# Optimization experiments

Measured on AMD Instinct MI355X. Metric: run time of the kernel, lower is better.

Reference implementation:

```python
import jax, jax.numpy as jnp
import numpy as np

V, K, D, T, B, M = 32000, 32, 256, 128, 128, 16
NEG = -1e9


def setup_inputs():
    key = jax.random.key(0)
    ks = jax.random.split(key, 32)
    def rn(k, shape):
        return (0.05 * jax.random.normal(k, shape)).astype(jnp.float32)
    u = jax.random.uniform(ks[4], (T, B, K), minval=1e-6, maxval=1.0 - 1e-6)
    return dict(
        keys=jax.random.randint(ks[0], (B, M), 1, V),
        vals=jax.random.randint(ks[1], (B, M), 1, V),
        sentences=jax.random.randint(ks[2], (B, T), 1, V),
        sent_lens=jax.random.randint(ks[3], (B,), T // 2, T + 1),
        tau=jnp.float32(0.5),
        x_lambd=jnp.float32(0.5),
        gumbel_noise=(-jnp.log(-jnp.log(u))).astype(jnp.float32),
        drop_unif=jax.random.uniform(ks[5], (B, T)).astype(jnp.float32),
        emb=rn(ks[6], (V, D)), z_emb=rn(ks[7], (K, D)),
        enc_Wih=rn(ks[8], (D, 4 * D)), enc_Whh=rn(ks[9], (D, 4 * D)), enc_b=jnp.zeros((4 * D,), jnp.float32),
        crf_W=rn(ks[10], (D, K)), crf_b=jnp.zeros((K,), jnp.float32), crf_trans=rn(ks[11], (K, K)),
        init_Wh=rn(ks[12], (D, D)), init_bh=jnp.zeros((D,), jnp.float32),
        init_Wc=rn(ks[13], (D, D)), init_bc=jnp.zeros((D,), jnp.float32),
        dec_Wih=rn(ks[14], (D, 4 * D)), dec_Whh=rn(ks[15], (D, 4 * D)), dec_b=jnp.zeros((4 * D,), jnp.float32),
        attn_Wq=rn(ks[16], (D, D)), attn_Wk=rn(ks[17], (D, D)), attn_v=rn(ks[18], (D,)),
        attn_out_W=rn(ks[19], (2 * D, D)), attn_out_b=jnp.zeros((D,), jnp.float32),
        pz_W=rn(ks[20], (D, K)), pz_b=jnp.zeros((K,), jnp.float32),
        int_W=rn(ks[21], (2 * D, D)), int_b=jnp.zeros((D,), jnp.float32),
        out_W=rn(ks[22], (D, V)), out_b=jnp.zeros((V,), jnp.float32),
        cattn_Wq=rn(ks[23], (D, D)), cattn_Wk=rn(ks[24], (D, D)), cattn_v=rn(ks[25], (D,)),
        g_W=rn(ks[26], (D, 1)), g_b=jnp.zeros((1,), jnp.float32),
    )


def _lstm_step(h, c, x, Wih, Whh, b):
    g = x @ Wih + h @ Whh + b
    i, f, gg, o = jnp.split(g, 4, axis=-1)
    c = jax.nn.sigmoid(f) * c + jax.nn.sigmoid(i) * jnp.tanh(gg)
    h = jax.nn.sigmoid(o) * jnp.tanh(c)
    return h, c


def _attend(q, memk, mem_vals, mask, v):
    # additive attention: q [B,D], memk = mem @ Wk [B,M,D]
    e = jnp.einsum('bmd,d->bm', jnp.tanh(q[:, None, :] + memk), v)
    e = jnp.where(mask, e, NEG)
    a = jax.nn.softmax(e, axis=-1)
    ctx = jnp.einsum('bm,bmd->bd', a, mem_vals)
    return ctx, a


def _forward(tau, x_lambd, gumbel_noise, drop_unif, emb, z_emb,
             enc_Wih, enc_Whh, enc_b, crf_W, crf_b, crf_trans,
             init_Wh, init_bh, init_Wc, init_bc,
             dec_Wih, dec_Whh, dec_b,
             attn_Wq, attn_Wk, attn_v, attn_out_W, attn_out_b,
             pz_W, pz_b, int_W, int_b, out_W, out_b,
             cattn_Wq, cattn_Wk, cattn_v, g_W, g_b,
             keys, vals, sentences, sent_lens):
    z_beta = 1.0
    lens = sent_lens
    # ---- q encoder: 1-layer LSTM over sentence embeddings ----
    sent_emb = emb[sentences]                            # [B,T,D]
    def enc_step(carry, x_t):
        h, c = _lstm_step(carry[0], carry[1], x_t, enc_Wih, enc_Whh, enc_b)
        return (h, c), h
    z0 = jnp.zeros((B, D), jnp.float32)
    _, enc_out = jax.lax.scan(enc_step, (z0, z0), sent_emb.transpose(1, 0, 2))
    enc_out = enc_out.transpose(1, 0, 2)                 # [B,T,D]
    # ---- emission scores with overlap logits ----
    phi = enc_out @ crf_W + crf_b                        # [B,T,K]
    phi = phi.at[:, :-1].add(phi[:, 1:])                 # scores[:,:-1] += scores[:,1:].clone()
    phi = phi.at[:, 1:].add(phi[:, :-1])                 # scores[:,1:]  += scores[:,:-1].clone()
    # ---- linear-chain CRF forward recursion: alpha + exact entropy ----
    phiT = phi.transpose(1, 0, 2)                        # [T,B,K]
    def crf_step(carry, inputs):
        alpha, H = carry
        phi_t, t = inputs
        scores = alpha[:, :, None] + crf_trans[None]     # [B,Ki,Kj]
        lZ = jax.nn.logsumexp(scores, axis=1)            # [B,Kj]
        logw = scores - lZ[:, None, :]
        w = jnp.exp(logw)
        na = lZ + phi_t
        nH = jnp.sum(w * (H[:, :, None] - logw), axis=1)
        m = (t < lens)[:, None]
        na = jnp.where(m, na, alpha)
        nH = jnp.where(m, nH, H)
        return (na, nH), na
    (aT, HT), alphas = jax.lax.scan(
        crf_step, (phiT[0], jnp.zeros((B, K), jnp.float32)),
        (phiT[1:], jnp.arange(1, T)))
    alphas = jnp.concatenate([phiT[0][None], alphas], axis=0)   # [T,B,K]
    logp_last = jax.nn.log_softmax(aT, axis=-1)
    ent_z = jnp.mean(jnp.sum(jnp.exp(logp_last) * (HT - logp_last), axis=-1))
    # ---- Gumbel FFBS backward sampling ----
    def bwd_step(nid, inputs):
        alpha_t, g_t, t = inputs
        is_last = (t == lens - 1)[:, None]
        active = (t < lens)
        logits = jnp.where(is_last, alpha_t, alpha_t + crf_trans[:, nid].T)
        y = jax.nn.softmax((logits + g_t) / tau, axis=-1)
        y = jnp.where(active[:, None], y, 0.0)
        ids = jnp.where(active, jnp.argmax(y, axis=-1).astype(jnp.int32), 0)
        return ids, (ids, y)
    ts = jnp.arange(T)
    _, (ids_r, y_r) = jax.lax.scan(
        bwd_step, jnp.zeros((B,), jnp.int32),
        (alphas[::-1], gumbel_noise[::-1], ts[::-1]))
    z_ids = ids_r[::-1].transpose(1, 0)                  # [B,T]
    z_sample = y_r[::-1].transpose(1, 0, 2)              # [B,T,K]
    z_sample_emb = z_sample @ z_emb                      # soft gumbel encode [B,T,D]
    # ---- key-value table encoding ----
    kv_mask = keys != 0
    kv_emb = emb[keys] + emb[vals]                       # [B,M,D]
    kvm = kv_mask.astype(jnp.float32)
    kv_enc = (kv_emb * kvm[..., None]).sum(1) / kvm.sum(1, keepdims=True)
    # ---- decoder io (word dropout x_lambd, z[0] zeroed) ----
    zse = z_sample_emb.at[:, 0].multiply(0.0)
    wmask = (drop_unif > x_lambd).astype(jnp.float32)[..., None]
    dec_inputs = (zse + sent_emb * wmask)[:, :-1]        # [B,T-1,D]
    tgt_x = sentences[:, 1:]
    tgt_z = z_ids[:, 1:]
    z_next = z_sample_emb[:, 1:]
    h0 = kv_enc @ init_Wh + init_bh
    c0 = kv_enc @ init_Wc + init_bc
    memk = kv_emb @ attn_Wk
    memk2 = kv_emb @ cattn_Wk
    rows = jnp.arange(B)
    def dec_step(carry, inputs):
        h, c = carry
        x_t, zn_t, tx, tz = inputs
        h, c = _lstm_step(h, c, x_t, dec_Wih, dec_Whh, dec_b)
        ctx, _ = _attend(h @ attn_Wq, memk, kv_emb, kv_mask, attn_v)
        dec_out = jnp.concatenate([h, ctx], axis=-1) @ attn_out_W + attn_out_b
        z_logits = dec_out @ pz_W + pz_b
        lpz = jnp.take_along_axis(jax.nn.log_softmax(z_logits, -1), tz[:, None], 1)[:, 0]
        dec_int = jnp.concatenate([dec_out, zn_t], axis=-1) @ int_W + int_b
        lm_prob = jax.nn.softmax(dec_int @ out_W + out_b, axis=-1)       # [B,V]
        _, copy_dist = _attend(dec_int @ cattn_Wq, memk2, kv_emb, kv_mask, cattn_v)
        copy_prob = jnp.zeros((B, V), lm_prob.dtype).at[rows[:, None], keys].add(copy_dist)
        g = jax.nn.sigmoid(dec_int @ g_W + g_b)                           # [B,1]
        out_prob = (1.0 - g) * lm_prob + g * copy_prob
        lpx = jnp.log(jnp.take_along_axis(out_prob, tx[:, None], 1)[:, 0] + 1e-10)
        return (h, c), (lpx, lpz)
    _, (lpx, lpz) = jax.lax.scan(
        dec_step, (h0, c0),
        (dec_inputs.transpose(1, 0, 2), z_next.transpose(1, 0, 2),
         tgt_x.transpose(1, 0), tgt_z.transpose(1, 0)))
    steps = jnp.arange(T - 1)
    smask = (steps[None, :] < lens[:, None]).astype(jnp.float32)
    denom = jnp.sum(lens).astype(jnp.float32)
    p_log_prob = (jnp.sum(lpx.transpose(1, 0) * smask) + jnp.sum(lpz.transpose(1, 0) * smask)) / denom
    loss = -(z_beta * ent_z + p_log_prob)
    return loss


def reference(keys, vals, sentences, sent_lens, tau, x_lambd, gumbel_noise,
              drop_unif, emb, z_emb, enc_Wih, enc_Whh, enc_b, crf_W, crf_b,
              crf_trans, init_Wh, init_bh, init_Wc, init_bc, dec_Wih, dec_Whh,
              dec_b, attn_Wq, attn_Wk, attn_v, attn_out_W, attn_out_b, pz_W,
              pz_b, int_W, int_b, out_W, out_b, cattn_Wq, cattn_Wk, cattn_v,
              g_W, g_b):
    return _forward(tau, x_lambd, gumbel_noise, drop_unif, emb, z_emb,
                    enc_Wih, enc_Whh, enc_b, crf_W, crf_b, crf_trans,
                    init_Wh, init_bh, init_Wc, init_bc, dec_Wih, dec_Whh,
                    dec_b, attn_Wq, attn_Wk, attn_v, attn_out_W, attn_out_b,
                    pz_W, pz_b, int_W, int_b, out_W, out_b,
                    cattn_Wq, cattn_Wk, cattn_v, g_W, g_b,
                    keys, vals, sentences, sent_lens)
```

## Files before the change

### kernel.cpp

```cpp
#include <hip/hip_runtime.h>
#include <math.h>

namespace {

constexpr int V_  = 32000;
constexpr int K_  = 32;
constexpr int D_  = 256;
constexpr int T_  = 128;
constexpr int B_  = 128;
constexpr int M_  = 16;
constexpr int D4_ = 1024;
constexpr int TD_ = T_ - 1;
constexpr int R_  = B_ * TD_;
constexpr int NCH_ = 8;

typedef __attribute__((ext_vector_type(8))) short short8;
typedef __attribute__((ext_vector_type(4))) float f32x4;
typedef __attribute__((ext_vector_type(2))) float f32x2;

__device__ __forceinline__ float d_rcp(float x){
#if __has_builtin(__builtin_amdgcn_rcpf)
  return __builtin_amdgcn_rcpf(x);
#else
  return 1.0f / x;
#endif
}
__device__ __forceinline__ float d_sig(float x){
  return d_rcp(1.0f + __expf(-x));
}
__device__ __forceinline__ float d_tanh(float x){
  float e = __expf(2.0f*x);
  return 1.0f - 2.0f*d_rcp(e + 1.0f);
}
__device__ __forceinline__ unsigned short f2bf(float f){
  unsigned int x = __float_as_uint(f);
  unsigned int r = (x + 0x7FFFu + ((x>>16)&1u)) >> 16;
  return (unsigned short)r;
}
__device__ __forceinline__ float bflo(unsigned u){ return __uint_as_float(u<<16); }
__device__ __forceinline__ float bfhi(unsigned u){ return __uint_as_float(u & 0xffff0000u); }

__device__ __forceinline__ unsigned f2fp8(float f){
  unsigned u = __float_as_uint(f);
  unsigned s = (u>>31)<<7;
  float a = fabsf(f);
  if (a < 0.015625f){
    int m = (int)rintf(a*512.0f);
    if (m >= 8) return s | 0x08u;
    return s | (unsigned)m;
  }
  unsigned t = u & 0x7FFFFFFFu;
  t += 0x7FFFFu + ((t>>20)&1u);
  int E = (int)(t>>23) - 127 + 7;
  if (E >= 16) return s | 0x7Eu;
  return s | ((unsigned)E<<3) | ((t>>20)&7u);
}

__device__ __forceinline__ unsigned pack4_fp8(float a, float b, float c, float d){
#if __has_builtin(__builtin_amdgcn_cvt_pk_fp8_f32)
  unsigned r = (unsigned)__builtin_amdgcn_cvt_pk_fp8_f32(a, b, 0, false);
  r = (unsigned)__builtin_amdgcn_cvt_pk_fp8_f32(c, d, (int)r, true);
  return r;
#else
  return f2fp8(a) | (f2fp8(b)<<8) | (f2fp8(c)<<16) | (f2fp8(d)<<24);
#endif
}
__device__ __forceinline__ unsigned char f2fp8_b(float f){
#if __has_builtin(__builtin_amdgcn_cvt_pk_fp8_f32)
  return (unsigned char)(__builtin_amdgcn_cvt_pk_fp8_f32(f, f, 0, false) & 0xFF);
#else
  return (unsigned char)f2fp8(f);
#endif
}

__device__ __forceinline__ void cvt4_fp8(unsigned w, float* o){
#if __has_builtin(__builtin_amdgcn_cvt_pk_f32_fp8)
  f32x2 lo = __builtin_amdgcn_cvt_pk_f32_fp8(w, false);
  f32x2 hi = __builtin_amdgcn_cvt_pk_f32_fp8(w, true);
  o[0]=lo.x; o[1]=lo.y; o[2]=hi.x; o[3]=hi.y;
#else
  #pragma unroll
  for (int j = 0; j < 4; j++){
    unsigned b = (w>>(8*j)) & 0xFFu;
    unsigned e = (b>>3) & 15u, m = b & 7u;
    float mag = e ? __uint_as_float(((e+120u)<<23)|(m<<20)) : (float)m*0.001953125f;
    o[j] = (b & 0x80u) ? -mag : mag;
  }
#endif
}

__global__ void k_sent_emb(const int* __restrict__ sent, const float* __restrict__ emb,
                           float* __restrict__ out){
  int idx = blockIdx.x*256 + threadIdx.x;
  int bt = idx >> 8, d = idx & 255;
  out[idx] = emb[(size_t)sent[bt]*D_ + d];
}

__global__ void k_kv_emb(const int* __restrict__ keys, const int* __restrict__ vals,
                         const float* __restrict__ emb, float* __restrict__ kv){
  int idx = blockIdx.x*256 + threadIdx.x;
  int r = idx >> 8, d = idx & 255;
  kv[idx] = emb[(size_t)keys[r]*D_ + d] + emb[(size_t)vals[r]*D_ + d];
}

__global__ void k_kv_enc(const int* __restrict__ keys, const float* __restrict__ kv,
                         float* __restrict__ out){
  int idx = blockIdx.x*256 + threadIdx.x;
  int b = idx >> 8, d = idx & 255;
  float s = 0.0f, c = 0.0f;
  for (int m = 0; m < M_; m++){
    if (keys[b*M_+m] != 0){ s += kv[(size_t)(b*M_+m)*D_ + d]; c += 1.0f; }
  }
  out[idx] = s / c;
}

__global__ void k_rowgemm(const float* __restrict__ A, const float* __restrict__ W,
                          const float* __restrict__ bias, float* __restrict__ C,
                          int inner, int cols){
  __shared__ float sA[256];
  int r = blockIdx.x;
  if ((int)threadIdx.x < inner) sA[threadIdx.x] = A[(size_t)r*inner + threadIdx.x];
  __syncthreads();
  for (int j = threadIdx.x; j < cols; j += blockDim.x){
    float acc = bias ? bias[j] : 0.0f;
    #pragma unroll 4
    for (int d = 0; d < inner; d++) acc += sA[d]*W[(size_t)d*cols + j];
    C[(size_t)r*cols + j] = acc;
  }
}

__global__ __launch_bounds__(256) void k_wt8(const float* __restrict__ W,
                                             unsigned char* __restrict__ Wt8, int ldw){
  __shared__ unsigned char st[64][272];
  int tid = threadIdx.x; size_t c0 = (size_t)blockIdx.x*64;
  for (int l = tid; l < 64*256; l += 256){
    int k = l >> 6, c = l & 63;
    st[c][k] = f2fp8_b(W[(size_t)k*ldw + c0 + c]);
  }
  __syncthreads();
  for (int l = tid; l < 64*16; l += 256){
    int c = l >> 4, s = l & 15;
    *reinterpret_cast<uint4*>(&Wt8[(c0+c)*256 + s*16]) =
      *reinterpret_cast<const uint4*>(&st[c][s*16]);
  }
}

__global__ __launch_bounds__(256) void k_wtg(const float* __restrict__ W,
                                             unsigned short* __restrict__ Wt, int ldw){
  __shared__ unsigned short st[64][264];
  int tid = threadIdx.x; size_t c0 = (size_t)blockIdx.x*64;
  for (int l = tid; l < 64*256; l += 256){
    int k = l >> 6, c = l & 63;
    st[c][k] = f2bf(W[(size_t)k*ldw + c0 + c]);
  }
  __syncthreads();
  for (int l = tid; l < 64*32; l += 256){
    int c = l >> 5, s = l & 31;
    *reinterpret_cast<uint4*>(&Wt[(c0+c)*256 + s*8]) =
      *reinterpret_cast<const uint4*>(&st[c][s*8]);
  }
}

__global__ __launch_bounds__(256) void k_wtg6(
    const float* s0, const float* s1, const float* s2,
    const float* s3, const float* s4, const float* s5,
    unsigned short* d0, unsigned short* d1, unsigned short* d2,
    unsigned short* d3, unsigned short* d4, unsigned short* d5){
  __shared__ unsigned short st[64][264];
  int m = blockIdx.x >> 2, blk = blockIdx.x & 3;
  const float* S; unsigned short* D;
  if      (m == 0){ S = s0; D = d0; }
  else if (m == 1){ S = s1; D = d1; }
  else if (m == 2){ S = s2; D = d2; }
  else if (m == 3){ S = s3; D = d3; }
  else if (m == 4){ S = s4; D = d4; }
  else            { S = s5; D = d5; }
  int tid = threadIdx.x; size_t c0 = (size_t)blk*64;
  for (int l = tid; l < 64*256; l += 256){
    int k = l >> 6, c = l & 63;
    st[c][k] = f2bf(S[(size_t)k*256 + c0 + c]);
  }
  __syncthreads();
  for (int l = tid; l < 64*32; l += 256){
    int c = l >> 5, s = l & 31;
    *reinterpret_cast<uint4*>(&D[(c0+c)*256 + s*8]) =
      *reinterpret_cast<const uint4*>(&st[c][s*8]);
  }
}

template<int G1, int G2, int HALVES, int CPB, bool BIAS, int TMD>
__global__ __launch_bounds__(512) void k_gemm(
    const float* __restrict__ A1, const float* __restrict__ A2,
    const unsigned short* __restrict__ W1, const unsigned short* __restrict__ W2,
    const float* __restrict__ bias, float* __restrict__ C, int cols,
    const float* __restrict__ drop, const float* __restrict__ xl){
  __shared__ unsigned short Al[128*256];
  __shared__ unsigned short Wl[64*256];
  int tid = threadIdx.x;
  int row0 = blockIdx.x*128;
  int w = tid >> 6, l = tid & 63;
  int arow = 16*w + (l & 15);
  float xlv = 0.0f;
  if constexpr (G1==1) xlv = xl[0];
  f32x4 acc[CPB][4];
  #pragma unroll
  for (int cc=0;cc<CPB;cc++)
    #pragma unroll
    for (int nf=0;nf<4;nf++) acc[cc][nf] = (f32x4){0.f,0.f,0.f,0.f};

  for (int h = 0; h < HALVES; h++){
    const float* Asrc = h ? A2 : A1;
    const unsigned short* Wt = h ? W2 : W1;
    int gm = h ? G2 : G1;
    __syncthreads();
    #pragma unroll
    for (int q = 0; q < 8; q++){
      int u = tid + q*512;
      int row = u >> 5, slot = u & 31;
      int r = row0 + row;
      float vals[8];
      if (gm == 0){
        const float* s = Asrc + (size_t)r*256 + slot*8;
        #pragma unroll
        for (int j=0;j<8;j++) vals[j] = s[j];
      } else if (gm == 1){
        int b = r / TD_, t = r - b*TD_;
        int bt = b*T_ + t;
        float wm = (drop[bt] > xlv) ? 1.0f : 0.0f;
        const float* se = A1 + (size_t)bt*256 + slot*8;
        const float* zs = A2 + (size_t)bt*256 + slot*8;
        #pragma unroll
        for (int j=0;j<8;j++) vals[j] = se[j]*wm + (t>0 ? zs[j] : 0.0f);
      } else {
        int b = r / TD_, t = r - b*TD_;
        const float* s = Asrc + (size_t)(b*T_ + t + 1)*256 + slot*8;
        #pragma unroll
        for (int j=0;j<8;j++) vals[j] = s[j];
      }
      union { unsigned short us[8]; uint4 v4; } tu;
      #pragma unroll
      for (int j=0;j<8;j++) tu.us[j] = f2bf(vals[j]);
// ... 38 lines not shown
  for (int cc = 0; cc < CPB; cc++){
    int col0 = (blockIdx.y*CPB + cc)*64;
    #pragma unroll
    for (int nf = 0; nf < 4; nf++){
      int col = col0 + nf*16 + (l & 15);
      float bv = BIAS ? bias[col] : 0.0f;
      #pragma unroll
      for (int r4 = 0; r4 < 4; r4++){
        int row = row0 + 16*w + (l>>4)*4 + r4;
        size_t orow;
        if constexpr (TMD == 0){
          orow = (size_t)row;
        } else {
          int bb = row / TMD, tt = row - bb*TMD;
          orow = (size_t)tt*B_ + bb;
        }
        C[orow*cols + col] = acc[cc][nf][r4] + bv;
      }
    }
  }
}

__global__ __launch_bounds__(1024, 4) void k_lstm12(
    const float* __restrict__ xW,
    const unsigned char* __restrict__ Wt,
    const float* __restrict__ h0, const float* __restrict__ c0,
    float* __restrict__ Hout,
    int NT){
  __shared__ unsigned char Wl[512*256];
  __shared__ unsigned char Ahl[2][16*256];
  int g0 = blockIdx.x;
  int tid = threadIdx.x;
  int w = tid >> 6, l = tid & 63;

  for (int i = tid; i < 512*16; i += 1024){
    int c = i >> 4, s16 = i & 15;
    int dst = c*256 + ((s16*16) ^ ((c&7)<<4));
    *reinterpret_cast<uint4*>(&Wl[dst]) =
      *reinterpret_cast<const uint4*>(&Wt[(size_t)c*256 + s16*16]);
  }
  if (tid < 256){
    int row = tid >> 4, gblk = tid & 15;
    unsigned pk[4];
    #pragma unroll
    for (int g = 0; g < 4; g++){
      float v0 = h0 ? h0[(size_t)(g0*16+row)*256 + gblk*16 + 4*g + 0] : 0.0f;
      float v1 = h0 ? h0[(size_t)(g0*16+row)*256 + gblk*16 + 4*g + 1] : 0.0f;
      float v2 = h0 ? h0[(size_t)(g0*16+row)*256 + gblk*16 + 4*g + 2] : 0.0f;
      float v3 = h0 ? h0[(size_t)(g0*16+row)*256 + gblk*16 + 4*g + 3] : 0.0f;
      pk[g] = pack4_fp8(v0, v1, v2, v3);
    }
    int dst = row*256 + ((gblk*16) ^ ((row&7)<<4));
    *reinterpret_cast<uint4*>(&Ahl[0][dst]) = *reinterpret_cast<const uint4*>(pk);
  }
  int cb = 16*w + (l & 15);
  int arow = l & 15;
  float creg[4];
  #pragma unroll
  for (int r = 0; r < 4; r++)
    creg[r] = c0 ? c0[(size_t)(g0*16 + (l>>4)*4 + r)*256 + cb] : 0.0f;

  int aoff[8], b0off[8], b1off[8];
  #pragma unroll
  for (int k0 = 0; k0 < 8; k0++){
    int kb = k0*32 + ((l>>4)*8);
    aoff[k0]  = arow*256 + (kb ^ ((arow&7)<<4));
    b0off[k0] = cb*256 + (kb ^ ((cb&7)<<4));
    b1off[k0] = (256+cb)*256 + (kb ^ ((cb&7)<<4));
  }
  const unsigned char* wg2 = Wt + (size_t)(512+cb)*256 + ((l>>4)*8);
  const unsigned char* wg3 = Wt + (size_t)(768+cb)*256 + ((l>>4)*8);
  int astore[4];
  const float* xb[4];
  float* hp[4];
  #pragma unroll
  for (int r = 0; r < 4; r++){
    int batch = (l>>4)*4 + r;
    astore[r] = batch*256 + ((cb & 0xF0) ^ ((batch&7)<<4)) + (cb & 15);
    xb[r] = xW + (size_t)(g0*16 + batch)*1024 + cb;
    hp[r] = Hout + (size_t)(g0*16 + batch)*NT*256 + cb;
  }
  __syncthreads();

  float xn[4][4];
  #pragma unroll
  for (int gt = 0; gt < 4; gt++)
    #pragma unroll
    for (int r = 0; r < 4; r++)
      xn[gt][r] = xb[r][gt*256];

  for (int t = 0; t < NT; t++){
    int cur = t & 1, nxt = cur ^ 1;
    f32x4 acc[4];
    #pragma unroll
    for (int gt = 0; gt < 4; gt++)
      #pragma unroll
      for (int r = 0; r < 4; r++)
        acc[gt][r] = xn[gt][r];
    if (t + 1 < NT){
      #pragma unroll
      for (int r = 0; r < 4; r++) xb[r] += B_*1024;
      #pragma unroll
      for (int gt = 0; gt < 4; gt++)
        #pragma unroll
        for (int r = 0; r < 4; r++)
          xn[gt][r] = xb[r][gt*256];
    }
    const unsigned char* Ac = Ahl[cur];
    #pragma unroll
    for (int k0 = 0; k0 < 8; k0++){
      long long afr = *reinterpret_cast<const long long*>(Ac + aoff[k0]);
      long long b0 = *reinterpret_cast<const long long*>(Wl + b0off[k0]);
      long long b1 = *reinterpret_cast<const long long*>(Wl + b1off[k0]);
      long long b2 = *reinterpret_cast<const long long*>(wg2 + k0*32);
      long long b3 = *reinterpret_cast<const long long*>(wg3 + k0*32);
      acc[0] = __builtin_amdgcn_mfma_f32_16x16x32_fp8_fp8(afr, b0, acc[0], 0, 0, 0);
      acc[1] = __builtin_amdgcn_mfma_f32_16x16x32_fp8_fp8(afr, b1, acc[1], 0, 0, 0);
      acc[2] = __builtin_amdgcn_mfma_f32_16x16x32_fp8_fp8(afr, b2, acc[2], 0, 0, 0);
      acc[3] = __builtin_amdgcn_mfma_f32_16x16x32_fp8_fp8(afr, b3, acc[3], 0, 0, 0);
    }
    #pragma unroll
    for (int r = 0; r < 4; r++){
      float vi = acc[0][r], vf = acc[1][r];
      float vg = acc[2][r], vo = acc[3][r];
      float cn = d_sig(vf)*creg[r] + d_sig(vi)*d_tanh(vg);
      float hn = d_sig(vo)*d_tanh(cn);
      creg[r] = cn;
      Ahl[nxt][astore[r]] = f2fp8_b(hn);
      hp[r][0] = hn;
      hp[r] += 256;
    }
    __syncthreads();
  }
}

__global__ __launch_bounds__(256) void k_phi(const float* __restrict__ H,
    const float* __restrict__ Wc, const float* __restrict__ bc,
    float* __restrict__ phi){
  int tid = threadIdx.x; int rl = tid >> 5, j = tid & 31;
  int r = blockIdx.x*8 + rl;
  int b = r >> 7, t = r & 127;
  float acc = bc[j];
  #pragma unroll 4
  for (int d = 0; d < 256; d++) acc += H[(size_t)r*256 + d]*Wc[d*K_ + j];
  phi[(size_t)t*B_*K_ + b*K_ + j] = acc;
}

__global__ __launch_bounds__(256) void k_zlp(const float* __restrict__ A,
    const float* __restrict__ Wz, const float* __restrict__ bz,
    const int* __restrict__ zids, float* __restrict__ lpz){
  int tid = threadIdx.x; int rl = tid >> 5, j = tid & 31;
  int r = blockIdx.x*8 + rl;
  float acc = bz[j];
  #pragma unroll 4
  for (int d = 0; d < 256; d++) acc += A[(size_t)r*256 + d]*Wz[d*K_ + j];
  float m = acc;
  #pragma unroll
  for (int off=16; off; off>>=1) m = fmaxf(m, __shfl_xor(m, off, 32));
  float e = __expf(acc - m), E = e;
  #pragma unroll
  for (int off=16; off; off>>=1) E += __shfl_xor(E, off, 32);
  int b = r / TD_, t = r - b*TD_;
  int tz = zids[b*T_ + t + 1];
  float vtz = __shfl(acc, tz, 32);
  if (j == 0) lpz[r] = vtz - (m + logf(E));
}

__global__ __launch_bounds__(1024) void k_crf(
    const float* __restrict__ phi, const float* __restrict__ trans,
    const int* __restrict__ lens, float* __restrict__ alphas,
    float* __restrict__ ent_b){
  __shared__ float sal[K_], sH[K_];
  int tid = threadIdx.x, b = blockIdx.x;
  int i = tid & 31, j = tid >> 5;
  float tr = trans[i*K_ + j];
  int len = lens[b];
  if (tid < K_){
    float a0 = phi[b*K_ + tid] + phi[(size_t)B_*K_ + b*K_ + tid];
    sal[tid] = a0; sH[tid] = 0.0f;
    alphas[b*K_ + tid] = a0;
  }
  __syncthreads();
  for (int t = 1; t < T_; t++){
    bool active = (t < len);
    float ai = sal[i], Hi = sH[i];
    float aj = sal[j], Hj = sH[j];
    float s = ai + tr;
    float m = s;
    #pragma unroll
    for (int off=16; off; off>>=1) m = fmaxf(m, __shfl_xor(m, off, 32));
    float e = expf(s - m);
    float E = e;
    #pragma unroll
    for (int off=16; off; off>>=1) E += __shfl_xor(E, off, 32);
    float lZ = m + logf(E);
    float w = e / E;
    float logw = s - lZ;
    float nH = w * (Hi - logw);
    #pragma unroll
    for (int off=16; off; off>>=1) nH += __shfl_xor(nH, off, 32);
    float pm = phi[(size_t)(t-1)*B_*K_ + b*K_ + j];
    float pt = phi[(size_t)t*B_*K_ + b*K_ + j];
    float ps = (t == T_-1) ? (pm + 2.0f*pt)
                           : (pm + 2.0f*pt + phi[(size_t)(t+1)*B_*K_ + b*K_ + j]);
    float na = lZ + ps;
    float outa = active ? na : aj;
    float outH = active ? nH : Hj;
    __syncthreads();
    if (i == 0){
      sal[j] = outa; sH[j] = outH;
      alphas[(size_t)t*B_*K_ + b*K_ + j] = outa;
    }
    __syncthreads();
  }
  if (tid < K_){
    float a = sal[tid];
    float m = a;
    #pragma unroll
    for (int off=16; off; off>>=1) m = fmaxf(m, __shfl_xor(m, off, 32));
    float e = expf(a-m), E = e;
    #pragma unroll
    for (int off=16; off; off>>=1) E += __shfl_xor(E, off, 32);
    float lse = m + logf(E);
    float lp = a - lse;
    float v = expf(lp)*(sH[tid]-lp);
    #pragma unroll
    for (int off=16; off; off>>=1) v += __shfl_xor(v, off, 32);
    if (tid == 0) ent_b[b] = v;
  }
}

__global__ void k_sampler(const float* __restrict__ alphas, const float* __restrict__ trans,
                          const float* __restrict__ gum, const int* __restrict__ lens,
                          const float* __restrict__ tau_p,
                          float* __restrict__ y_all, int* __restrict__ z_ids){
  int b = blockIdx.x;
  int lane = threadIdx.x;
  int k = lane & 31;
  float inv_tau = d_rcp(tau_p[0]);
  int len = lens[b];
  int nid = 0;
  for (int t = T_-1; t >= 0; t--){
    bool active  = (t < len);
    bool is_last = (t == len-1);
    float a = alphas[(size_t)t*B_*K_ + b*K_ + k];
    float lg = is_last ? a : a + trans[k*K_ + nid];
    float val = (lg + gum[(size_t)t*B_*K_ + b*K_ + k]) * inv_tau;
    float m = val;
    #pragma unroll
    for (int off=16; off; off>>=1) m = fmaxf(m, __shfl_xor(m, off, 32));
    float e = expf(val - m), E = e;
    #pragma unroll
    for (int off=16; off; off>>=1) E += __shfl_xor(E, off, 32);
    float y = active ? e*d_rcp(E) : 0.0f;
    if (lane < K_) y_all[(size_t)(b*T_ + t)*K_ + k] = y;
    float bv = val; int bk = k;
    #pragma unroll
    for (int off=16; off; off>>=1){
      float ov = __shfl_xor(bv, off, 32);
      int   ok = __shfl_xor(bk, off, 32);
      if (ov > bv || (ov == bv && ok < bk)){ bv = ov; bk = ok; }
    }
    int ids = active ? bk : 0;
    nid = ids;
    if (lane == 0) z_ids[b*T_ + t] = ids;
  }
}

__global__ __launch_bounds__(256) void k_attn1(
    const float* __restrict__ q, const float* __restrict__ memk,
    const float* __restrict__ kv_emb, const int* __restrict__ keys,
    const float* __restrict__ av, float* __restrict__ ctx){
  __shared__ float se[16];
  int r = blockIdx.x, tid = threadIdx.x;
  int b = r / TD_;
  int m = tid >> 4, ds = tid & 15;
  float p = 0.0f;
  #pragma unroll 4
  for (int qq = 0; qq < 16; qq++){
    int dd = ds + qq*16;
    p += d_tanh(q[(size_t)r*256 + dd] + memk[(size_t)(b*M_+m)*256 + dd]) * av[dd];
  }
  #pragma unroll
  for (int off=8; off; off>>=1) p += __shfl_xor(p, off, 16);
  if (ds == 0) se[m] = (keys[b*M_+m] != 0) ? p : -1e9f;
  __syncthreads();
  float mx = -1e30f;
  #pragma unroll
  for (int mm=0;mm<16;mm++) mx = fmaxf(mx, se[mm]);
  float den = 0.0f, ex[16];
  #pragma unroll
  for (int mm=0;mm<16;mm++){ ex[mm] = __expf(se[mm]-mx); den += ex[mm]; }
  float cacc = 0.0f;
  #pragma unroll
  for (int mm=0;mm<16;mm++) cacc += ex[mm]*kv_emb[(size_t)(b*M_+mm)*256 + tid];
  ctx[(size_t)r*256 + tid] = cacc*d_rcp(den);
}

__global__ __launch_bounds__(256) void k_attn2g(
    const float* __restrict__ q2, const float* __restrict__ dint,
    const float* __restrict__ memk2, const int* __restrict__ keys,
    const float* __restrict__ cv, const float* __restrict__ gW, const float* __restrict__ gb,
    const int* __restrict__ sent,
    float* __restrict__ cpx, float* __restrict__ gsig){
  __shared__ float se2[16];
  __shared__ float sred[4];
  int r = blockIdx.x, tid = threadIdx.x;
  int b = r / TD_, t = r - b*TD_;
  int m = tid >> 4, ds = tid & 15;
  float p = 0.0f;
  #pragma unroll 4
  for (int qq = 0; qq < 16; qq++){
    int dd = ds + qq*16;
    p += d_tanh(q2[(size_t)r*256 + dd] + memk2[(size_t)(b*M_+m)*256 + dd]) * cv[dd];
  }
  #pragma unroll
  for (int off=8; off; off>>=1) p += __shfl_xor(p, off, 16);
  if (ds == 0) se2[m] = (keys[b*M_+m] != 0) ? p : -1e9f;
  float gp = dint[(size_t)r*256 + tid]*gW[tid];
  #pragma unroll
  for (int off=32; off; off>>=1) gp += __shfl_xor(gp, off, 64);
  if ((tid & 63) == 0) sred[tid>>6] = gp;
  __syncthreads();
  if (tid == 0){
    float mx = -1e30f;
    #pragma unroll
    for (int mm=0;mm<16;mm++) mx = fmaxf(mx, se2[mm]);
    float den = 0.0f, ex[16];
    #pragma unroll
    for (int mm=0;mm<16;mm++){ ex[mm] = __expf(se2[mm]-mx); den += ex[mm]; }
    int txi = sent[b*T_ + t + 1];
    float idn = d_rcp(den);
    float cp = 0.0f;
    #pragma unroll
    for (int mm=0;mm<16;mm++) if (keys[b*M_+mm] == txi) cp += ex[mm]*idn;
    cpx[r] = cp;
    gsig[r] = d_sig(sred[0]+sred[1]+sred[2]+sred[3] + gb[0]);
  }
}

__global__ __launch_bounds__(512) void k_lse8(
    const float* __restrict__ Af,
    const unsigned char* __restrict__ Wt8,
    const float* __restrict__ bias,
    float* __restrict__ part){
  __shared__ unsigned char Al[256*256];
  __shared__ unsigned char Wl[64*256];
  int tid = threadIdx.x;
  int row0 = blockIdx.x*256;
  #pragma unroll
  for (int q = 0; q < 8; q++){
    int u = tid + q*512;
    int row = u >> 4, s16 = u & 15;
    int r = row0 + row;
    unsigned pk[4] = {0u,0u,0u,0u};
    if (r < R_){
      const float* src = Af + (size_t)r*256 + s16*16;
      #pragma unroll
      for (int g = 0; g < 4; g++){
        float4 f = *reinterpret_cast<const float4*>(src + g*4);
        pk[g] = pack4_fp8(f.x, f.y, f.z, f.w);
      }
    }
    int dst = row*256 + ((s16*16) ^ ((row&7)<<4));
    *reinterpret_cast<uint4*>(&Al[dst]) = *reinterpret_cast<const uint4*>(pk);
  }
  __syncthreads();
  int w = tid >> 6, l = tid & 63;
  int arow = 16*w + (l & 15);
  long long afrA[8], afrB[8];
  #pragma unroll
  for (int k0 = 0; k0 < 8; k0++){
    int kb = k0*32 + ((l>>4)*8);
    afrA[k0] = *reinterpret_cast<const long long*>(&Al[arow*256 + (kb ^ ((arow&7)<<4))]);
    int ar2 = arow + 128;
    afrB[k0] = *reinterpret_cast<const long long*>(&Al[ar2*256 + (kb ^ ((ar2&7)<<4))]);
  }
  float rm[2][4], rs[2][4];
  #pragma unroll
  for (int rf=0;rf<2;rf++)
    #pragma unroll
    for (int r4=0;r4<4;r4++){ rm[rf][r4] = -3.0e38f; rs[rf][r4] = 0.0f; }

  for (int ct = blockIdx.y; ct < 500; ct += NCH_){
    int col0 = ct*64;
    __syncthreads();
    #pragma unroll
    for (int q = 0; q < 2; q++){
      int u = tid + q*512;
      int c = u >> 4, s16 = u & 15;
      int dst = c*256 + ((s16*16) ^ ((c&7)<<4));
      *reinterpret_cast<uint4*>(&Wl[dst]) =
        *reinterpret_cast<const uint4*>(&Wt8[(size_t)(col0+c)*256 + s16*16]);
    }
    __syncthreads();
    f32x4 acc[2][4];
    #pragma unroll
    for (int rf=0;rf<2;rf++)
      #pragma unroll
      for (int nf=0;nf<4;nf++) acc[rf][nf] = (f32x4){0.f,0.f,0.f,0.f};
    #pragma unroll
    for (int k0 = 0; k0 < 8; k0++){
      int kb = k0*32 + ((l>>4)*8);
      #pragma unroll
      for (int nf = 0; nf < 4; nf++){
        int bc = nf*16 + (l & 15);
        long long bfr = *reinterpret_cast<const long long*>(&Wl[bc*256 + (kb ^ ((bc&7)<<4))]);
        acc[0][nf] = __builtin_amdgcn_mfma_f32_16x16x32_fp8_fp8(afrA[k0], bfr, acc[0][nf], 0, 0, 0);
        acc[1][nf] = __builtin_amdgcn_mfma_f32_16x16x32_fp8_fp8(afrB[k0], bfr, acc[1][nf], 0, 0, 0);
      }
    }
    float bb[4];
    #pragma unroll
    for (int nf=0;nf<4;nf++) bb[nf] = bias[col0 + nf*16 + (l&15)];
    #pragma unroll
    for (int rf = 0; rf < 2; rf++){
      #pragma unroll
      for (int r4 = 0; r4 < 4; r4++){
        float v0 = acc[rf][0][r4]+bb[0], v1 = acc[rf][1][r4]+bb[1];
        float v2 = acc[rf][2][r4]+bb[2], v3 = acc[rf][3][r4]+bb[3];
        float tm = fmaxf(fmaxf(v0,v1), fmaxf(v2,v3));
        float ts = __expf(v0-tm)+__expf(v1-tm)+__expf(v2-tm)+__expf(v3-tm);
        float m0 = rm[rf][r4];
        if (tm <= m0){
          rs[rf][r4] += ts*__expf(tm - m0);
        } else {
          rs[rf][r4] = rs[rf][r4]*__expf(m0 - tm) + ts;
          rm[rf][r4] = tm;
        }
      }
    }
  }
  #pragma unroll
  for (int rf = 0; rf < 2; rf++){
    #pragma unroll
    for (int r4 = 0; r4 < 4; r4++){
      float M = rm[rf][r4];
      #pragma unroll
      for (int off=8; off; off>>=1) M = fmaxf(M, __shfl_xor(M, off, 16));
      float S = rs[rf][r4]*__expf(rm[rf][r4] - M);
      #pragma unroll
      for (int off=8; off; off>>=1) S += __shfl_xor(S, off, 16);
      if ((l & 15) == 0){
        int grow = row0 + rf*128 + 16*w + (l>>4)*4 + r4;
        if (grow < R_){
          part[((size_t)grow*NCH_ + blockIdx.y)*2 + 0] = M;
          part[((size_t)grow*NCH_ + blockIdx.y)*2 + 1] = S;
        }
      }
    }
  }
}

__global__ void k_lse_combine(const float* __restrict__ part, float* __restrict__ lse){
  int r = blockIdx.x*256 + threadIdx.x;
  if (r >= R_) return;
  float M = -3.0e38f;
  for (int c = 0; c < NCH_; c++) M = fmaxf(M, part[((size_t)r*NCH_+c)*2]);
  float S = 0.0f;
  for (int c = 0; c < NCH_; c++){
    float m = part[((size_t)r*NCH_+c)*2], s = part[((size_t)r*NCH_+c)*2+1];
    S += s*__expf(m - M);
  }
  lse[r] = M + logf(S);
}

__global__ __launch_bounds__(256) void k_ltx(const float* __restrict__ dint,
    const unsigned char* __restrict__ Wt8, const float* __restrict__ bias,
    const int* __restrict__ sent, float* __restrict__ out){
  int tid = threadIdx.x;
  int r = blockIdx.x*4 + (tid >> 6);
  int lane = tid & 63;
  int b = r / TD_, t = r - b*TD_;
  int tx = sent[b*T_ + t + 1];
  unsigned wq = *reinterpret_cast<const unsigned*>(Wt8 + (size_t)tx*256 + lane*4);
  float wv[4]; cvt4_fp8(wq, wv);
  const float* ap = dint + (size_t)r*256 + lane*4;
  unsigned aq = pack4_fp8(ap[0], ap[1], ap[2], ap[3]);
  float av[4]; cvt4_fp8(aq, av);
  float acc = av[0]*wv[0] + av[1]*wv[1] + av[2]*wv[2] + av[3]*wv[3];
  #pragma unroll
  for (int off=32; off; off>>=1) acc += __shfl_xor(acc, off, 64);
  if (lane == 0) out[r] = acc + bias[tx];
}

__global__ __launch_bounds__(256) void k_final(
    const float* __restrict__ lse, const float* __restrict__ ltx,
    const float* __restrict__ gsig, const float* __restrict__ cpx,
    const float* __restrict__ lpz, const float* __restrict__ ent_b,
    const int* __restrict__ lens, float* __restrict__ out){
  __shared__ float sred[256];
  int tid = threadIdx.x;
  float sum = 0.0f;
  for (int r = tid; r < R_; r += 256){
    int b = r / TD_, t = r % TD_;
    if (t < lens[b]){
      float g = gsig[r];
      float lm = __expf(ltx[r] - lse[r]);
      float p = (1.0f-g)*lm + g*cpx[r] + 1e-10f;
      sum += logf(p) + lpz[r];
    }
  }
  sred[tid] = sum;
  __syncthreads();
  for (int s = 128; s; s >>= 1){ if (tid < s) sred[tid] += sred[tid+s]; __syncthreads(); }
  if (tid == 0){
    float es = 0.0f, dn = 0.0f;
    for (int b = 0; b < B_; b++){ es += ent_b[b]; dn += (float)lens[b]; }
    out[0] = -( es/(float)B_ + sred[0]/dn );
  }
}

}

// ... 3 lines not shown
  const int*   keys  = (const int*)d_in[0];
  const int*   vals  = (const int*)d_in[1];
  const int*   sent  = (const int*)d_in[2];
  const int*   lens  = (const int*)d_in[3];
  const float* tau   = (const float*)d_in[4];
  const float* xl    = (const float*)d_in[5];
  const float* gum   = (const float*)d_in[6];
  const float* drop  = (const float*)d_in[7];
  const float* emb   = (const float*)d_in[8];
  const float* z_emb = (const float*)d_in[9];
  const float* eWih  = (const float*)d_in[10];
  const float* eWhh  = (const float*)d_in[11];
  const float* eb    = (const float*)d_in[12];
  const float* crfW  = (const float*)d_in[13];
  const float* crfb  = (const float*)d_in[14];
  const float* trans = (const float*)d_in[15];
  const float* iWh   = (const float*)d_in[16];
  const float* ibh   = (const float*)d_in[17];
  const float* iWc   = (const float*)d_in[18];
  const float* ibc   = (const float*)d_in[19];
  const float* dWih  = (const float*)d_in[20];
  const float* dWhh  = (const float*)d_in[21];
  const float* db    = (const float*)d_in[22];
  const float* aWq   = (const float*)d_in[23];
  const float* aWk   = (const float*)d_in[24];
  const float* av    = (const float*)d_in[25];
  const float* aoW   = (const float*)d_in[26];
  const float* aob   = (const float*)d_in[27];
  const float* pzW   = (const float*)d_in[28];
  const float* pzb   = (const float*)d_in[29];
  const float* intW  = (const float*)d_in[30];
  const float* intb  = (const float*)d_in[31];
  const float* outW  = (const float*)d_in[32];
  const float* outb  = (const float*)d_in[33];
  const float* cWq   = (const float*)d_in[34];
  const float* cWk   = (const float*)d_in[35];
  const float* cv    = (const float*)d_in[36];
  const float* gW    = (const float*)d_in[37];
  const float* gb    = (const float*)d_in[38];
  (void)in_sizes; (void)n_in; (void)out_size; (void)ws_size;

  float* ws = (float*)d_ws;
  size_t o = 0;
  auto alloc = [&](size_t n){ size_t r = o; o += (n + 3) & ~(size_t)3; return r; };
  float* sent_emb = ws + alloc((size_t)B_*T_*D_);
  float* kv_emb   = ws + alloc((size_t)B_*M_*D_);
  float* kv_enc   = ws + alloc((size_t)B_*D_);
  float* h0       = ws + alloc((size_t)B_*D_);
  float* c0       = ws + alloc((size_t)B_*D_);
  float* memk     = ws + alloc((size_t)B_*M_*D_);
  float* memk2    = ws + alloc((size_t)B_*M_*D_);
  float* xW       = ws + alloc((size_t)B_*T_*D4_);
  float* encH     = ws + alloc((size_t)B_*T_*D_);
  float* phi_raw  = ws + alloc((size_t)T_*B_*K_);
  float* alphas   = ws + alloc((size_t)T_*B_*K_);
  float* ent_b    = ws + alloc((size_t)B_);
  float* y_all    = ws + alloc((size_t)B_*T_*K_);
  float* zse      = ws + alloc((size_t)B_*T_*D_);
  float* qbuf     = ws + alloc((size_t)R_*D_);
  float* ctx      = ws + alloc((size_t)R_*D_);
  float* dec_out  = ws + alloc((size_t)R_*D_);
  float* dint     = ws + alloc((size_t)R_*D_);
  float* lpz_b    = ws + alloc((size_t)R_);
  float* gsig     = ws + alloc((size_t)R_);
  float* cpx      = ws + alloc((size_t)R_);
  float* ltx      = ws + alloc((size_t)R_);
  float* lse      = ws + alloc((size_t)R_);
  float* part     = ws + alloc((size_t)R_*NCH_*2);
  int*   z_ids    = (int*)(ws + alloc((size_t)B_*T_));
  unsigned char* WhhT8E = (unsigned char*)(ws + alloc((size_t)D4_*D_/4));
  unsigned char* WhhT8D = (unsigned char*)(ws + alloc((size_t)D4_*D_/4));
  unsigned char* Wt8    = (unsigned char*)(ws + alloc((size_t)V_*D_/4));
  unsigned short* eWihT = (unsigned short*)(ws + alloc((size_t)D4_*D_/2));
  unsigned short* dWihT = (unsigned short*)(ws + alloc((size_t)D4_*D_/2));
  unsigned short* aWqT  = (unsigned short*)(ws + alloc((size_t)D_*D_/2));
  unsigned short* cWqT  = (unsigned short*)(ws + alloc((size_t)D_*D_/2));
  unsigned short* aoWtT = (unsigned short*)(ws + alloc((size_t)D_*D_/2));
  unsigned short* aoWbT = (unsigned short*)(ws + alloc((size_t)D_*D_/2));
  unsigned short* inWtT = (unsigned short*)(ws + alloc((size_t)D_*D_/2));
  unsigned short* inWbT = (unsigned short*)(ws + alloc((size_t)D_*D_/2));

  float* Hdec = encH;

  k_sent_emb<<<B_*T_*D_/256, 256, 0, stream>>>(sent, emb, sent_emb);
  k_kv_emb  <<<B_*M_*D_/256, 256, 0, stream>>>(keys, vals, emb, kv_emb);
  k_kv_enc  <<<B_*D_/256, 256, 0, stream>>>(keys, kv_emb, kv_enc);
  k_rowgemm <<<B_,     256, 0, stream>>>(kv_enc, iWh, ibh, h0, 256, 256);
  k_rowgemm <<<B_,     256, 0, stream>>>(kv_enc, iWc, ibc, c0, 256, 256);
  k_rowgemm <<<B_*M_,  256, 0, stream>>>(kv_emb, aWk, nullptr, memk, 256, 256);
  k_rowgemm <<<B_*M_,  256, 0, stream>>>(kv_emb, cWk, nullptr, memk2, 256, 256);
  k_wt8<<<D4_/64, 256, 0, stream>>>(eWhh, WhhT8E, D4_);
  k_wt8<<<D4_/64, 256, 0, stream>>>(dWhh, WhhT8D, D4_);
  k_wt8<<<V_/64, 256, 0, stream>>>(outW, Wt8, V_);
  k_wtg<<<16, 256, 0, stream>>>(eWih, eWihT, D4_);
  k_wtg<<<16, 256, 0, stream>>>(dWih, dWihT, D4_);
  k_wtg6<<<24, 256, 0, stream>>>(aWq, cWq, aoW, aoW + 256*256, intW, intW + 256*256,
                                 aWqT, cWqT, aoWtT, aoWbT, inWtT, inWbT);

  k_gemm<0,0,1,4,true,T_><<<dim3(B_*T_/128, 4), 512, 0, stream>>>(
      sent_emb, nullptr, eWihT, nullptr, eb, xW, D4_, nullptr, nullptr);
  k_lstm12<<<B_/16, 1024, 0, stream>>>(xW, WhhT8E, nullptr, nullptr, encH, T_);
  k_phi<<<B_*T_/8, 256, 0, stream>>>(encH, crfW, crfb, phi_raw);
  k_crf<<<B_, 1024, 0, stream>>>(phi_raw, trans, lens, alphas, ent_b);
  k_sampler<<<B_, 64, 0, stream>>>(alphas, trans, gum, lens, tau, y_all, z_ids);
  k_rowgemm<<<B_*T_, 256, 0, stream>>>(y_all, z_emb, nullptr, zse, K_, 256);

  k_gemm<1,0,1,4,true,TD_><<<dim3(R_/128, 4), 512, 0, stream>>>(
      sent_emb, zse, dWihT, nullptr, db, xW, D4_, drop, xl);
  k_lstm12<<<B_/16, 1024, 0, stream>>>(xW, WhhT8D, h0, c0, Hdec, TD_);

  k_gemm<0,0,1,1,false,0><<<dim3(R_/128, 4), 512, 0, stream>>>(
      Hdec, nullptr, aWqT, nullptr, nullptr, qbuf, D_, nullptr, nullptr);
  k_attn1<<<R_, 256, 0, stream>>>(qbuf, memk, kv_emb, keys, av, ctx);
  k_gemm<0,0,2,1,true,0><<<dim3(R_/128, 4), 512, 0, stream>>>(
      Hdec, ctx, aoWtT, aoWbT, aob, dec_out, D_, nullptr, nullptr);
  k_zlp<<<R_/8, 256, 0, stream>>>(dec_out, pzW, pzb, z_ids, lpz_b);
  k_gemm<0,2,2,1,true,0><<<dim3(R_/128, 4), 512, 0, stream>>>(
      dec_out, zse, inWtT, inWbT, intb, dint, D_, nullptr, nullptr);
  k_gemm<0,0,1,1,false,0><<<dim3(R_/128, 4), 512, 0, stream>>>(
      dint, nullptr, cWqT, nullptr, nullptr, qbuf, D_, nullptr, nullptr);
  k_attn2g<<<R_, 256, 0, stream>>>(qbuf, dint, memk2, keys, cv, gW, gb, sent,
                                   cpx, gsig);

  k_lse8<<<dim3((R_+255)/256, NCH_), 512, 0, stream>>>(dint, Wt8, outb, part);
  k_lse_combine<<<(R_+255)/256, 256, 0, stream>>>(part, lse);
  k_ltx<<<R_/4, 256, 0, stream>>>(dint, Wt8, outb, sent, ltx);
  k_final<<<1, 256, 0, stream>>>(lse, ltx, gsig, cpx, lpz_b, ent_b, lens, (float*)d_out);
}
```

Baseline: 1.812 ms.

## Fuse setup kernels, double-buffer CRF and logit weight tiles, streamline LSTM gates

Merges the embedding gathers, the paired row GEMMs and the paired weight-transpose kernels into single launches to cut launch overhead. The CRF forward loop now double-buffers its shared alpha/entropy arrays, dropping one barrier per step. The vocabulary logit kernel double-buffers its fp8 weight tile in shared memory with a register prefetch two tiles ahead, overlapping global loads with MFMA work. The LSTM recurrence alternates between two accumulator sets and rewrites the gate math to use fewer reciprocals, at some cost in register pressure and a small change in rounding.

```diff
diff --git a/kernel.cpp b/kernel.cpp
--- a/kernel.cpp
+++ b/kernel.cpp
@@ -37,8 +37,6 @@
   unsigned int r = (x + 0x7FFFu + ((x>>16)&1u)) >> 16;
   return (unsigned short)r;
 }
-__device__ __forceinline__ float bflo(unsigned u){ return __uint_as_float(u<<16); }
-__device__ __forceinline__ float bfhi(unsigned u){ return __uint_as_float(u & 0xffff0000u); }
 
 __device__ __forceinline__ unsigned f2fp8(float f){
   unsigned u = __float_as_uint(f);
@@ -89,18 +87,17 @@
 #endif
 }
 
-__global__ void k_sent_emb(const int* __restrict__ sent, const float* __restrict__ emb,
-                           float* __restrict__ out){
-  int idx = blockIdx.x*256 + threadIdx.x;
-  int bt = idx >> 8, d = idx & 255;
-  out[idx] = emb[(size_t)sent[bt]*D_ + d];
-}
-
-__global__ void k_kv_emb(const int* __restrict__ keys, const int* __restrict__ vals,
-                         const float* __restrict__ emb, float* __restrict__ kv){
-  int idx = blockIdx.x*256 + threadIdx.x;
-  int r = idx >> 8, d = idx & 255;
-  kv[idx] = emb[(size_t)keys[r]*D_ + d] + emb[(size_t)vals[r]*D_ + d];
+__global__ void k_emb2(const int* __restrict__ sent, const int* __restrict__ keys,
+                       const int* __restrict__ vals, const float* __restrict__ emb,
+                       float* __restrict__ sent_emb, float* __restrict__ kv){
+  int bid = blockIdx.x, tid = threadIdx.x;
+  if (bid < B_*T_){
+    sent_emb[(size_t)bid*256 + tid] = emb[(size_t)sent[bid]*D_ + tid];
+  } else {
+    int r = bid - B_*T_;
+    kv[(size_t)r*256 + tid] = emb[(size_t)keys[r]*D_ + tid]
+                            + emb[(size_t)vals[r]*D_ + tid];
+  }
 }
 
 __global__ void k_kv_enc(const int* __restrict__ keys, const float* __restrict__ kv,
@@ -129,6 +126,29 @@
   }
 }
 
+__global__ void k_rowgemm2(const float* __restrict__ A,
+                           const float* __restrict__ W1, const float* __restrict__ b1,
+                           float* __restrict__ C1,
+                           const float* __restrict__ W2, const float* __restrict__ b2,
+                           float* __restrict__ C2, int inner, int cols){
+  __shared__ float sA[256];
+  int r = blockIdx.x;
+  if ((int)threadIdx.x < inner) sA[threadIdx.x] = A[(size_t)r*inner + threadIdx.x];
+  __syncthreads();
+  for (int j = threadIdx.x; j < cols; j += blockDim.x){
+    float a1 = b1 ? b1[j] : 0.0f;
+    float a2 = b2 ? b2[j] : 0.0f;
+    #pragma unroll 4
+    for (int d = 0; d < inner; d++){
+      float a = sA[d];
+      a1 += a*W1[(size_t)d*cols + j];
+      a2 += a*W2[(size_t)d*cols + j];
+    }
+    C1[(size_t)r*cols + j] = a1;
+    C2[(size_t)r*cols + j] = a2;
+  }
+}
+
 __global__ __launch_bounds__(256) void k_wt8(const float* __restrict__ W,
                                              unsigned char* __restrict__ Wt8, int ldw){
   __shared__ unsigned char st[64][272];
@@ -145,10 +165,32 @@
   }
 }
 
-__global__ __launch_bounds__(256) void k_wtg(const float* __restrict__ W,
-                                             unsigned short* __restrict__ Wt, int ldw){
+__global__ __launch_bounds__(256) void k_wt8_2(const float* __restrict__ W1,
+    const float* __restrict__ W2, unsigned char* __restrict__ O1,
+    unsigned char* __restrict__ O2, int ldw){
+  __shared__ unsigned char st[64][272];
+  const float* W = (blockIdx.x < 16) ? W1 : W2;
+  unsigned char* O = (blockIdx.x < 16) ? O1 : O2;
+  int tid = threadIdx.x; size_t c0 = (size_t)(blockIdx.x & 15)*64;
+  for (int l = tid; l < 64*256; l += 256){
+    int k = l >> 6, c = l & 63;
+    st[c][k] = f2fp8_b(W[(size_t)k*ldw + c0 + c]);
+  }
+  __syncthreads();
+  for (int l = tid; l < 64*16; l += 256){
+    int c = l >> 4, s = l & 15;
+    *reinterpret_cast<uint4*>(&O[(c0+c)*256 + s*16]) =
+      *reinterpret_cast<const uint4*>(&st[c][s*16]);
+  }
+}
+
+__global__ __launch_bounds__(256) void k_wtg2(const float* __restrict__ W1,
+    const float* __restrict__ W2, unsigned short* __restrict__ O1,
+    unsigned short* __restrict__ O2, int ldw){
   __shared__ unsigned short st[64][264];
-  int tid = threadIdx.x; size_t c0 = (size_t)blockIdx.x*64;
+  const float* W = (blockIdx.x < 16) ? W1 : W2;
+  unsigned short* O = (blockIdx.x < 16) ? O1 : O2;
+  int tid = threadIdx.x; size_t c0 = (size_t)(blockIdx.x & 15)*64;
   for (int l = tid; l < 64*256; l += 256){
     int k = l >> 6, c = l & 63;
     st[c][k] = f2bf(W[(size_t)k*ldw + c0 + c]);
@@ -156,7 +198,7 @@
   __syncthreads();
   for (int l = tid; l < 64*32; l += 256){
     int c = l >> 5, s = l & 31;
-    *reinterpret_cast<uint4*>(&Wt[(c0+c)*256 + s*8]) =
+    *reinterpret_cast<uint4*>(&O[(c0+c)*256 + s*8]) =
       *reinterpret_cast<const uint4*>(&st[c][s*8]);
   }
 }
@@ -361,21 +403,14 @@
   }
   __syncthreads();
 
-  float xn[4][4];
+  f32x4 accA[4], accB[4];
   #pragma unroll
   for (int gt = 0; gt < 4; gt++)
     #pragma unroll
     for (int r = 0; r < 4; r++)
-      xn[gt][r] = xb[r][gt*256];
-
-  for (int t = 0; t < NT; t++){
-    int cur = t & 1, nxt = cur ^ 1;
-    f32x4 acc[4];
-    #pragma unroll
-    for (int gt = 0; gt < 4; gt++)
-      #pragma unroll
-      for (int r = 0; r < 4; r++)
-        acc[gt][r] = xn[gt][r];
+      accA[gt][r] = xb[r][gt*256];
+
+  auto step = [&](f32x4 (&aC)[4], f32x4 (&aN)[4], int t){
     if (t + 1 < NT){
       #pragma unroll
       for (int r = 0; r < 4; r++) xb[r] += B_*1024;
@@ -383,9 +418,10 @@
       for (int gt = 0; gt < 4; gt++)
         #pragma unroll
         for (int r = 0; r < 4; r++)
-          xn[gt][r] = xb[r][gt*256];
-    }
-    const unsigned char* Ac = Ahl[cur];
+          aN[gt][r] = xb[r][gt*256];
+    }
+    const unsigned char* Ac = Ahl[t & 1];
+    unsigned char* An = Ahl[(t & 1) ^ 1];
     #pragma unroll
     for (int k0 = 0; k0 < 8; k0++){
       long long afr = *reinterpret_cast<const long long*>(Ac + aoff[k0]);
@@ -393,23 +429,34 @@
       long long b1 = *reinterpret_cast<const long long*>(Wl + b1off[k0]);
       long long b2 = *reinterpret_cast<const long long*>(wg2 + k0*32);
       long long b3 = *reinterpret_cast<const long long*>(wg3 + k0*32);
-      acc[0] = __builtin_amdgcn_mfma_f32_16x16x32_fp8_fp8(afr, b0, acc[0], 0, 0, 0);
-      acc[1] = __builtin_amdgcn_mfma_f32_16x16x32_fp8_fp8(afr, b1, acc[1], 0, 0, 0);
-      acc[2] = __builtin_amdgcn_mfma_f32_16x16x32_fp8_fp8(afr, b2, acc[2], 0, 0, 0);
-      acc[3] = __builtin_amdgcn_mfma_f32_16x16x32_fp8_fp8(afr, b3, acc[3], 0, 0, 0);
+      aC[0] = __builtin_amdgcn_mfma_f32_16x16x32_fp8_fp8(afr, b0, aC[0], 0, 0, 0);
+      aC[1] = __builtin_amdgcn_mfma_f32_16x16x32_fp8_fp8(afr, b1, aC[1], 0, 0, 0);
+      aC[2] = __builtin_amdgcn_mfma_f32_16x16x32_fp8_fp8(afr, b2, aC[2], 0, 0, 0);
+      aC[3] = __builtin_amdgcn_mfma_f32_16x16x32_fp8_fp8(afr, b3, aC[3], 0, 0, 0);
     }
     #pragma unroll
     for (int r = 0; r < 4; r++){
-      float vi = acc[0][r], vf = acc[1][r];
-      float vg = acc[2][r], vo = acc[3][r];
-      float cn = d_sig(vf)*creg[r] + d_sig(vi)*d_tanh(vg);
-      float hn = d_sig(vo)*d_tanh(cn);
+      float vi = aC[0][r], vf = aC[1][r];
+      float vg = aC[2][r], vo = aC[3][r];
+      float sf = d_rcp(1.0f + __expf(-vf));
+      float eg = __expf(2.0f*vg);
+      float di = 1.0f + __expf(-vi);
+      float term = (eg - 1.0f) * d_rcp(di*(eg + 1.0f));
+      float cn = sf*creg[r] + term;
+      float eo = 1.0f + __expf(-vo);
+      float ec = __expf(2.0f*cn);
+      float hn = (ec - 1.0f) * d_rcp(eo*(ec + 1.0f));
       creg[r] = cn;
-      Ahl[nxt][astore[r]] = f2fp8_b(hn);
+      An[astore[r]] = f2fp8_b(hn);
       hp[r][0] = hn;
       hp[r] += 256;
     }
     __syncthreads();
+  };
+
+  for (int t = 0; t < NT; t++){
+    if ((t & 1) == 0) step(accA, accB, t);
+    else              step(accB, accA, t);
   }
 }
 
@@ -449,21 +496,22 @@
     const float* __restrict__ phi, const float* __restrict__ trans,
     const int* __restrict__ lens, float* __restrict__ alphas,
     float* __restrict__ ent_b){
-  __shared__ float sal[K_], sH[K_];
+  __shared__ float sal[2][K_], sH[2][K_];
   int tid = threadIdx.x, b = blockIdx.x;
   int i = tid & 31, j = tid >> 5;
   float tr = trans[i*K_ + j];
   int len = lens[b];
   if (tid < K_){
     float a0 = phi[b*K_ + tid] + phi[(size_t)B_*K_ + b*K_ + tid];
-    sal[tid] = a0; sH[tid] = 0.0f;
+    sal[0][tid] = a0; sH[0][tid] = 0.0f;
     alphas[b*K_ + tid] = a0;
   }
   __syncthreads();
   for (int t = 1; t < T_; t++){
+    int cur = (t-1) & 1, nxt = t & 1;
     bool active = (t < len);
-    float ai = sal[i], Hi = sH[i];
-    float aj = sal[j], Hj = sH[j];
+    float ai = sal[cur][i], Hi = sH[cur][i];
+    float aj = sal[cur][j], Hj = sH[cur][j];
     float s = ai + tr;
     float m = s;
     #pragma unroll
@@ -485,15 +533,15 @@
     float na = lZ + ps;
     float outa = active ? na : aj;
     float outH = active ? nH : Hj;
+    if (i == 0){
+      sal[nxt][j] = outa; sH[nxt][j] = outH;
+      alphas[(size_t)t*B_*K_ + b*K_ + j] = outa;
+    }
     __syncthreads();
-    if (i == 0){
-      sal[j] = outa; sH[j] = outH;
-      alphas[(size_t)t*B_*K_ + b*K_ + j] = outa;
-    }
-    __syncthreads();
-  }
+  }
+  int fb = (T_-1) & 1;
   if (tid < K_){
-    float a = sal[tid];
+    float a = sal[fb][tid];
     float m = a;
     #pragma unroll
     for (int off=16; off; off>>=1) m = fmaxf(m, __shfl_xor(m, off, 32));
@@ -502,7 +550,7 @@
     for (int off=16; off; off>>=1) E += __shfl_xor(E, off, 32);
     float lse = m + logf(E);
     float lp = a - lse;
-    float v = expf(lp)*(sH[tid]-lp);
+    float v = expf(lp)*(sH[fb][tid]-lp);
     #pragma unroll
     for (int off=16; off; off>>=1) v += __shfl_xor(v, off, 32);
     if (tid == 0) ent_b[b] = v;
@@ -624,7 +672,7 @@
     const float* __restrict__ bias,
     float* __restrict__ part){
   __shared__ unsigned char Al[256*256];
-  __shared__ unsigned char Wl[64*256];
+  __shared__ unsigned char Wl[2][64*256];
   int tid = threadIdx.x;
   int row0 = blockIdx.x*256;
   #pragma unroll
@@ -661,18 +709,37 @@
     #pragma unroll
     for (int r4=0;r4<4;r4++){ rm[rf][r4] = -3.0e38f; rs[rf][r4] = 0.0f; }
 
-  for (int ct = blockIdx.y; ct < 500; ct += NCH_){
-    int col0 = ct*64;
-    __syncthreads();
-    #pragma unroll
-    for (int q = 0; q < 2; q++){
-      int u = tid + q*512;
-      int c = u >> 4, s16 = u & 15;
-      int dst = c*256 + ((s16*16) ^ ((c&7)<<4));
-      *reinterpret_cast<uint4*>(&Wl[dst]) =
-        *reinterpret_cast<const uint4*>(&Wt8[(size_t)(col0+c)*256 + s16*16]);
-    }
-    __syncthreads();
+  int s16 = tid & 15;
+  int c0q = tid >> 4;
+  int c1q = c0q + 32;
+  int src0 = c0q*256 + s16*16;
+  int src1 = c1q*256 + s16*16;
+  int dst0 = c0q*256 + ((s16*16) ^ ((c0q&7)<<4));
+  int dst1 = c1q*256 + ((s16*16) ^ ((c1q&7)<<4));
+  uint4 wr0, wr1;
+  int ct0 = blockIdx.y;
+  wr0 = *reinterpret_cast<const uint4*>(Wt8 + (size_t)ct0*16384 + src0);
+  wr1 = *reinterpret_cast<const uint4*>(Wt8 + (size_t)ct0*16384 + src1);
+  *reinterpret_cast<uint4*>(&Wl[0][dst0]) = wr0;
+  *reinterpret_cast<uint4*>(&Wl[0][dst1]) = wr1;
+  if (ct0 + NCH_ < 500){
+    wr0 = *reinterpret_cast<const uint4*>(Wt8 + (size_t)(ct0+NCH_)*16384 + src0);
+    wr1 = *reinterpret_cast<const uint4*>(Wt8 + (size_t)(ct0+NCH_)*16384 + src1);
+  }
+  __syncthreads();
+
+  int it = 0;
+  for (int ct = ct0; ct < 500; ct += NCH_, it++){
+    int cur = it & 1, nxt = cur ^ 1;
+    if (ct + NCH_ < 500){
+      *reinterpret_cast<uint4*>(&Wl[nxt][dst0]) = wr0;
+      *reinterpret_cast<uint4*>(&Wl[nxt][dst1]) = wr1;
+    }
+    if (ct + 2*NCH_ < 500){
+      wr0 = *reinterpret_cast<const uint4*>(Wt8 + (size_t)(ct+2*NCH_)*16384 + src0);
+      wr1 = *reinterpret_cast<const uint4*>(Wt8 + (size_t)(ct+2*NCH_)*16384 + src1);
+    }
+    const unsigned char* Wc = Wl[cur];
     f32x4 acc[2][4];
     #pragma unroll
     for (int rf=0;rf<2;rf++)
@@ -684,11 +751,12 @@
       #pragma unroll
       for (int nf = 0; nf < 4; nf++){
         int bc = nf*16 + (l & 15);
-        long long bfr = *reinterpret_cast<const long long*>(&Wl[bc*256 + (kb ^ ((bc&7)<<4))]);
+        long long bfr = *reinterpret_cast<const long long*>(&Wc[bc*256 + (kb ^ ((bc&7)<<4))]);
         acc[0][nf] = __builtin_amdgcn_mfma_f32_16x16x32_fp8_fp8(afrA[k0], bfr, acc[0][nf], 0, 0, 0);
         acc[1][nf] = __builtin_amdgcn_mfma_f32_16x16x32_fp8_fp8(afrB[k0], bfr, acc[1][nf], 0, 0, 0);
       }
     }
+    int col0 = ct*64;
     float bb[4];
     #pragma unroll
     for (int nf=0;nf<4;nf++) bb[nf] = bias[col0 + nf*16 + (l&15)];
@@ -709,6 +777,7 @@
         }
       }
     }
+    __syncthreads();
   }
   #pragma unroll
   for (int rf = 0; rf < 2; rf++){
@@ -878,18 +947,14 @@
 
   float* Hdec = encH;
 
-  k_sent_emb<<<B_*T_*D_/256, 256, 0, stream>>>(sent, emb, sent_emb);
-  k_kv_emb  <<<B_*M_*D_/256, 256, 0, stream>>>(keys, vals, emb, kv_emb);
-  k_kv_enc  <<<B_*D_/256, 256, 0, stream>>>(keys, kv_emb, kv_enc);
-  k_rowgemm <<<B_,     256, 0, stream>>>(kv_enc, iWh, ibh, h0, 256, 256);
-  k_rowgemm <<<B_,     256, 0, stream>>>(kv_enc, iWc, ibc, c0, 256, 256);
-  k_rowgemm <<<B_*M_,  256, 0, stream>>>(kv_emb, aWk, nullptr, memk, 256, 256);
-  k_rowgemm <<<B_*M_,  256, 0, stream>>>(kv_emb, cWk, nullptr, memk2, 256, 256);
-  k_wt8<<<D4_/64, 256, 0, stream>>>(eWhh, WhhT8E, D4_);
-  k_wt8<<<D4_/64, 256, 0, stream>>>(dWhh, WhhT8D, D4_);
+  k_emb2<<<B_*T_ + B_*M_, 256, 0, stream>>>(sent, keys, vals, emb, sent_emb, kv_emb);
+  k_kv_enc<<<B_*D_/256, 256, 0, stream>>>(keys, kv_emb, kv_enc);
+  k_rowgemm2<<<B_, 256, 0, stream>>>(kv_enc, iWh, ibh, h0, iWc, ibc, c0, 256, 256);
+  k_rowgemm2<<<B_*M_, 256, 0, stream>>>(kv_emb, aWk, nullptr, memk,
+                                        cWk, nullptr, memk2, 256, 256);
+  k_wt8_2<<<32, 256, 0, stream>>>(eWhh, dWhh, WhhT8E, WhhT8D, D4_);
   k_wt8<<<V_/64, 256, 0, stream>>>(outW, Wt8, V_);
-  k_wtg<<<16, 256, 0, stream>>>(eWih, eWihT, D4_);
-  k_wtg<<<16, 256, 0, stream>>>(dWih, dWihT, D4_);
+  k_wtg2<<<32, 256, 0, stream>>>(eWih, dWih, eWihT, dWihT, D4_);
   k_wtg6<<<24, 256, 0, stream>>>(aWq, cWq, aoW, aoW + 256*256, intW, intW + 256*256,
                                  aWqT, cWqT, aoWtT, aoWbT, inWtT, inWbT);
 
```

After: 3.430 ms. 89.3% more time.
